# Optimization experiments

Hardware: AMD Instinct MI355X
Metric: run time of the kernel (lower is better)

Reference implementation:

```python
import jax, jax.numpy as jnp
import numpy as np

EMBED = 1024
HEADS = 8
HEAD_DIM = EMBED // HEADS
WINDOW = 128
B, T = 2, 2048


def setup_inputs() -> dict:
    key = jax.random.key(0)
    ks = jax.random.split(key, 6)
    s_in = 1.0 / np.sqrt(EMBED)
    return {
        "x": jax.random.normal(ks[0], (B, T, EMBED), dtype=jnp.float32),
        "W_qkv": jax.random.normal(ks[1], (EMBED, 3 * EMBED), dtype=jnp.float32) * s_in,
        "b_qkv": jax.random.normal(ks[2], (3 * EMBED,), dtype=jnp.float32) * 0.01,
        "W_proj": jax.random.normal(ks[3], (EMBED, EMBED), dtype=jnp.float32) * s_in,
        "b_proj": jax.random.normal(ks[4], (EMBED,), dtype=jnp.float32) * 0.01,
        "gate": jnp.ones((EMBED,), dtype=jnp.float32),
    }


def reference(x, W_qkv, b_qkv, W_proj, b_proj, gate):
    Bb, Tt, C = x.shape
    qkv = x @ W_qkv + b_qkv                       # [B,T,3C]
    q, k, v = jnp.split(qkv, 3, axis=-1)
    # [B,H,T,D]
    q = q.reshape(Bb, Tt, HEADS, HEAD_DIM).transpose(0, 2, 1, 3)
    k = k.reshape(Bb, Tt, HEADS, HEAD_DIM).transpose(0, 2, 1, 3)
    v = v.reshape(Bb, Tt, HEADS, HEAD_DIM).transpose(0, 2, 1, 3)
    scale = 1.0 / np.sqrt(HEAD_DIM).astype(np.float32)
    att = jnp.einsum('bhqd,bhkd->bhqk', q, k) * scale
    idx = jnp.arange(Tt)
    # causal AND within |i-j| <= window  (diagonal always valid -> no all-masked rows)
    mask = (idx[:, None] >= idx[None, :]) & (jnp.abs(idx[:, None] - idx[None, :]) <= WINDOW)
    att = jnp.where(mask[None, None], att, -jnp.inf)
    att = jax.nn.softmax(att, axis=-1)
    out = jnp.einsum('bhqk,bhkd->bhqd', att, v)
    out = out.transpose(0, 2, 1, 3).reshape(Bb, Tt, C)
    return (out * gate) @ W_proj + b_proj
```

## Files before the change

### kernel.cpp

```cpp
#include <hip/hip_runtime.h>

typedef unsigned short u16;
typedef unsigned int u32;
typedef __attribute__((ext_vector_type(4))) float f32x4;
typedef __attribute__((ext_vector_type(8))) short bf16x8;
typedef __attribute__((ext_vector_type(8))) unsigned short u16x8;

#define SEQ   2048
#define NB    2
#define NH    8
#define HD    128
#define EMB   1024
#define WIN   128
#define MTOT  4096
#define NQKV  3072
#define HSZ   (SEQ*HD)
#define QKVSZ (NB*NH*HSZ)

static __device__ __forceinline__ u16 f2bf(float f){
  u32 x = __builtin_bit_cast(u32, f);
  x += 0x7fffu + ((x >> 16) & 1u);
  return (u16)(x >> 16);
}

static __device__ __forceinline__ void gload_lds16(const void* g, void* l){
  __builtin_amdgcn_global_load_lds((__attribute__((address_space(1))) void*)(void*)(g),
                                   (__attribute__((address_space(3))) void*)(l), 16, 0, 0);
}


__global__ __launch_bounds__(256) void cvt_bf16(const float* __restrict__ in,
                                                u16* __restrict__ out, int n){
  int i = (blockIdx.x * 256 + threadIdx.x) * 8;
  const int stride = gridDim.x * 256 * 8;
  for (; i < n; i += stride){
    float4 a = *(const float4*)(in + i);
    float4 b = *(const float4*)(in + i + 4);
    uint4 o;
    o.x = (u32)f2bf(a.x) | ((u32)f2bf(a.y) << 16);
    o.y = (u32)f2bf(a.z) | ((u32)f2bf(a.w) << 16);
    o.z = (u32)f2bf(b.x) | ((u32)f2bf(b.y) << 16);
    o.w = (u32)f2bf(b.z) | ((u32)f2bf(b.w) << 16);
    *(uint4*)(out + i) = o;
  }
}

__global__ __launch_bounds__(256) void transpose_cvt(const float* __restrict__ in,
                                                     u16* __restrict__ out, int R, int C){
  __shared__ float tile[32][33];
  const int bx = blockIdx.x * 32;
  const int by = blockIdx.y * 32;
  const int tx = threadIdx.x & 31, ty = threadIdx.x >> 5;
  #pragma unroll
  for (int i = 0; i < 32; i += 8)
    tile[ty + i][tx] = in[(size_t)(by + ty + i) * C + bx + tx];
  __syncthreads();
  #pragma unroll
  for (int i = 0; i < 32; i += 8)
    out[(size_t)(bx + ty + i) * R + by + tx] = f2bf(tile[tx][ty + i]);
}


template<int EPIL>
__global__ __launch_bounds__(256) void gemm_bf16(
    const u16* __restrict__ A,
    const u16* __restrict__ Bt,
    const float* __restrict__ bias,
    u16* __restrict__ obf,
    float* __restrict__ of)
{
  constexpr int K = 1024, BK = 64;
  __shared__ u16 As[128 * 64];
  __shared__ u16 Bs[128 * 64];
  const int tid = threadIdx.x, lane = tid & 63, wave = tid >> 6;
  const int m0 = blockIdx.y * 128, n0 = blockIdx.x * 128;
  const int wr = (wave >> 1) * 64, wc = (wave & 1) * 64;

  const int srow = lane >> 3;
  const int scol = ((((lane & 7) << 4) ^ (srow << 4)) >> 1);
  const u16* ag = A  + (size_t)(m0 + wave * 32 + srow) * K + scol;
  const u16* bg = Bt + (size_t)(n0 + wave * 32 + srow) * K + scol;
  u16* al = &As[wave * 32 * 64];
  u16* bl = &Bs[wave * 32 * 64];

  f32x4 acc[4][4] = {};

  for (int kt = 0; kt < K / BK; ++kt){
    #pragma unroll
    for (int j = 0; j < 4; ++j){
      gload_lds16(ag + (size_t)j * 8 * K + kt * BK, al + j * 8 * 64);
      gload_lds16(bg + (size_t)j * 8 * K + kt * BK, bl + j * 8 * 64);
    }
    __syncthreads();
    #pragma unroll
    for (int ks = 0; ks < 2; ++ks){
      const int fr = lane & 15;
      const int colb = ((ks << 6) + ((lane >> 4) << 4)) ^ ((lane & 7) << 4);
      bf16x8 af[4], bfr[4];
      #pragma unroll
      for (int mi = 0; mi < 4; ++mi)
        af[mi] = *(const bf16x8*)((const char*)As + (wr + mi * 16 + fr) * 128 + colb);
      #pragma unroll
      for (int ni = 0; ni < 4; ++ni)
        bfr[ni] = *(const bf16x8*)((const char*)Bs + (wc + ni * 16 + fr) * 128 + colb);
      #pragma unroll
      for (int mi = 0; mi < 4; ++mi)
        #pragma unroll
        for (int ni = 0; ni < 4; ++ni)
          acc[mi][ni] = __builtin_amdgcn_mfma_f32_16x16x32_bf16(af[mi], bfr[ni], acc[mi][ni], 0, 0, 0);
    }
    __syncthreads();
  }

  #pragma unroll
  for (int mi = 0; mi < 4; ++mi){
    const int rg = m0 + wr + mi * 16 + ((lane >> 4) << 2);
    #pragma unroll
    for (int ni = 0; ni < 4; ++ni){
      const int cg = n0 + wc + ni * 16 + (lane & 15);
      const float bs = bias[cg];
      if constexpr (EPIL == 0){
        const int which = cg >> 10, hm = cg & 1023;
        const int b = rg >> 11, t = rg & 2047;
        u16* dst = obf + (size_t)which * QKVSZ
                       + ((size_t)(b * NH + (hm >> 7)) * SEQ + t) * HD + (hm & 127);
        #pragma unroll
        for (int j = 0; j < 4; ++j)
          dst[(size_t)j * HD] = f2bf(acc[mi][ni][j] + bs);
      } else {
        #pragma unroll
        for (int j = 0; j < 4; ++j)
          of[(size_t)(rg + j) * EMB + cg] = acc[mi][ni][j] + bs;
      }
    }
  }
}


__global__ __launch_bounds__(256) void attn_kernel(
    const u16* __restrict__ QKVb, const float* __restrict__ gate, u16* __restrict__ Ao)
{
  __shared__ float S[64 * 196];
  __shared__ u16 KV[128 * 72];
  const int tid = threadIdx.x, lane = tid & 63, wave = tid >> 6;
  const int q0 = blockIdx.x * 64;
  const int bh = blockIdx.y;
  const u16* Qg = QKVb + (size_t)bh * HSZ;
  const u16* Kg = QKVb + (size_t)QKVSZ + (size_t)bh * HSZ;
  const u16* Vg = QKVb + (size_t)2 * QKVSZ + (size_t)bh * HSZ;
  const int kstart = q0 - WIN;

  bf16x8 qf[4];
  {
    const u16* qp = Qg + (size_t)(q0 + wave * 16 + (lane & 15)) * HD + 8 * (lane >> 4);
    #pragma unroll
    for (int ks = 0; ks < 4; ++ks) qf[ks] = *(const bf16x8*)(qp + ks * 32);
  }
  const float scale = 0.08838834764831845f;

  for (int c = 0; c < 3; ++c){
    {
      const int keyl = tid >> 2;
      int krow = kstart + c * 64 + keyl;
      krow = min(max(krow, 0), SEQ - 1);
      const u16* kp = Kg + (size_t)krow * HD + (tid & 3) * 8;
      u16* ksh = &KV[keyl * 136 + (tid & 3) * 8];
      #pragma unroll
      for (int r = 0; r < 4; ++r)
        *(uint4*)(ksh + r * 32) = *(const uint4*)(kp + r * 32);
    }
    __syncthreads();
    f32x4 sacc[4] = {};
    #pragma unroll
    for (int ks = 0; ks < 4; ++ks){
      #pragma unroll
      for (int nf = 0; nf < 4; ++nf){
        bf16x8 kf = *(const bf16x8*)(&KV[(nf * 16 + (lane & 15)) * 136 + ks * 32 + 8 * (lane >> 4)]);
        sacc[nf] = __builtin_amdgcn_mfma_f32_16x16x32_bf16(qf[ks], kf, sacc[nf], 0, 0, 0);
      }
    }
    #pragma unroll
    for (int nf = 0; nf < 4; ++nf){
      const int kc = c * 64 + nf * 16 + (lane & 15);
      const int kg = kstart + kc;
      #pragma unroll
      for (int j = 0; j < 4; ++j){
        const int qr = wave * 16 + ((lane >> 4) << 2) + j;
        const int qg = q0 + qr;
        const bool ok = (kg >= 0) && (kg <= qg) && (qg - kg <= WIN);
        S[qr * 196 + kc] = ok ? sacc[nf][j] * scale : -1e30f;
      }
    }
    __syncthreads();
  }

  {
    const int r = tid >> 2, sub = tid & 3;
    float4 v[12];
    float mx = -1e30f;
    #pragma unroll
    for (int i = 0; i < 12; ++i){
      v[i] = *(const float4*)(&S[r * 196 + (sub + 4 * i) * 4]);
      mx = fmaxf(mx, fmaxf(fmaxf(v[i].x, v[i].y), fmaxf(v[i].z, v[i].w)));
    }
    mx = fmaxf(mx, __shfl_xor(mx, 1));
    mx = fmaxf(mx, __shfl_xor(mx, 2));
    float sum = 0.f;
    #pragma unroll
    for (int i = 0; i < 12; ++i){
      v[i].x = __expf(v[i].x - mx); v[i].y = __expf(v[i].y - mx);
      v[i].z = __expf(v[i].z - mx); v[i].w = __expf(v[i].w - mx);
      sum += v[i].x + v[i].y + v[i].z + v[i].w;
    }
    sum += __shfl_xor(sum, 1);
    sum += __shfl_xor(sum, 2);
    const float inv = 1.0f / sum;
    #pragma unroll
    for (int i = 0; i < 12; ++i){
      v[i].x *= inv; v[i].y *= inv; v[i].z *= inv; v[i].w *= inv;
      *(float4*)(&S[r * 196 + (sub + 4 * i) * 4]) = v[i];
    }
  }
  __syncthreads();

  f32x4 oacc[8] = {};
  for (int c = 0; c < 3; ++c){
    {
      const int keyl = tid & 63;
      int krow = kstart + c * 64 + keyl;
      krow = min(max(krow, 0), SEQ - 1);
      const u16* vp = Vg + (size_t)krow * HD + (tid >> 6) * 32;
      #pragma unroll
      for (int r2 = 0; r2 < 4; ++r2){
        u16x8 vv = *(const u16x8*)(vp + r2 * 8);
        const int dbase = (tid >> 6) * 32 + r2 * 8;
        #pragma unroll
        for (int j = 0; j < 8; ++j)
          KV[(dbase + j) * 72 + keyl] = vv[j];
      }
    }
    __syncthreads();
    #pragma unroll
    for (int ks = 0; ks < 2; ++ks){
      const float* sp = &S[(wave * 16 + (lane & 15)) * 196 + c * 64 + ks * 32 + 8 * (lane >> 4)];
      float4 p0 = *(const float4*)sp;
      float4 p1 = *(const float4*)(sp + 4);
      bf16x8 pf;
      pf[0] = (short)f2bf(p0.x); pf[1] = (short)f2bf(p0.y);
      pf[2] = (short)f2bf(p0.z); pf[3] = (short)f2bf(p0.w);
      pf[4] = (short)f2bf(p1.x); pf[5] = (short)f2bf(p1.y);
      pf[6] = (short)f2bf(p1.z); pf[7] = (short)f2bf(p1.w);
      #pragma unroll
      for (int nf = 0; nf < 8; ++nf){
        bf16x8 vf = *(const bf16x8*)(&KV[(nf * 16 + (lane & 15)) * 72 + ks * 32 + 8 * (lane >> 4)]);
        oacc[nf] = __builtin_amdgcn_mfma_f32_16x16x32_bf16(pf, vf, oacc[nf], 0, 0, 0);
      }
    }
    __syncthreads();
  }

  {
    const int b = bh >> 3, h = bh & 7;
    #pragma unroll
    for (int nf = 0; nf < 8; ++nf){
      const int d = nf * 16 + (lane & 15);
      const float gv = gate[h * HD + d];
      #pragma unroll
      for (int j = 0; j < 4; ++j){
        const int t = q0 + wave * 16 + ((lane >> 4) << 2) + j;
        Ao[((size_t)(b * SEQ + t)) * EMB + h * HD + d] = f2bf(oacc[nf][j] * gv);
      }
    }
  }
}


extern "C" void kernel_launch(void* const* d_in, const int* in_sizes, int n_in,
                              void* d_out, int out_size, void* d_ws, size_t ws_size,
                              hipStream_t stream)
{
  const float* x     = (const float*)d_in[0];
  const float* Wqkv  = (const float*)d_in[1];
  const float* bqkv  = (const float*)d_in[2];
  const float* Wproj = (const float*)d_in[3];
  const float* bproj = (const float*)d_in[4];
  const float* gate  = (const float*)d_in[5];
  float* out = (float*)d_out;

  u16* Xb   = (u16*)d_ws;
  u16* Wqt  = Xb   + (size_t)MTOT * EMB;
  u16* Wpt  = Wqt  + (size_t)NQKV * EMB;
  u16* QKVb = Wpt  + (size_t)EMB * EMB;
  u16* Ao   = QKVb + (size_t)3 * QKVSZ;

  cvt_bf16<<<dim3(2048), dim3(256), 0, stream>>>(x, Xb, MTOT * EMB);
  transpose_cvt<<<dim3(NQKV / 32, EMB / 32), dim3(256), 0, stream>>>(Wqkv, Wqt, EMB, NQKV);
  transpose_cvt<<<dim3(EMB / 32, EMB / 32), dim3(256), 0, stream>>>(Wproj, Wpt, EMB, EMB);

  gemm_bf16<0><<<dim3(NQKV / 128, MTOT / 128), dim3(256), 0, stream>>>(
      Xb, Wqt, bqkv, QKVb, (float*)nullptr);

  attn_kernel<<<dim3(SEQ / 64, NB * NH), dim3(256), 0, stream>>>(QKVb, gate, Ao);

  gemm_bf16<1><<<dim3(EMB / 128, MTOT / 128), dim3(256), 0, stream>>>(
      Ao, Wpt, bproj, (u16*)nullptr, out);
}
```

Before: 157.4 us.

## Replace QKV GEMM with 256x256 tiled, 8-wave, double-buffered pipelined kernel

Adds a dedicated QKV projection GEMM that uses 256x256 output tiles with 512 threads. Global-to-LDS loads are double-buffered and interleaved with MFMA phases, using explicit vmcnt waits, barriers and setprio. A grouped block-index swizzle is added for L2 locality. The goal is to raise data reuse per tile and overlap memory with compute in the largest GEMM. The cost is 128 KB of LDS per block and only 192 workgroups, which may underfill the GPU's compute units and risks ordering bugs in the hand-scheduled pipeline.

```diff
diff --git a/kernel.cpp b/kernel.cpp
--- a/kernel.cpp
+++ b/kernel.cpp
@@ -27,6 +27,8 @@
   __builtin_amdgcn_global_load_lds((__attribute__((address_space(1))) void*)(void*)(g),
                                    (__attribute__((address_space(3))) void*)(l), 16, 0, 0);
 }
+
+#define VMW(n) asm volatile("s_waitcnt vmcnt(" #n ")" ::: "memory")
 
 
 __global__ __launch_bounds__(256) void cvt_bf16(const float* __restrict__ in,
@@ -61,12 +63,130 @@
 }
 
 
-template<int EPIL>
-__global__ __launch_bounds__(256) void gemm_bf16(
+#define SLOTB 32768
+
+__global__ __launch_bounds__(512, 2) void gemm256_qkv(
     const u16* __restrict__ A,
     const u16* __restrict__ Bt,
     const float* __restrict__ bias,
-    u16* __restrict__ obf,
+    u16* __restrict__ obf)
+{
+  constexpr int K = 1024;
+  constexpr int NIT = K / 128;
+  __shared__ char sm[131072];
+  char* smA = sm;
+  char* smB = sm + 2 * SLOTB;
+
+  const int tid = threadIdx.x, lane = tid & 63, w = tid >> 6;
+  const int wr = w >> 2, wc = w & 3;
+  const int fr = lane & 15, hk = lane >> 4;
+
+  const int nwg = 16 * 12;
+  const int bid = blockIdx.x;
+  const int swz = (bid & 7) * (nwg >> 3) + (bid >> 3);
+  const int bx = swz % 12, by = swz / 12;
+  const int m0 = by * 256, n0 = bx * 256;
+
+  const int srow = lane >> 3;
+  const int scol = (((lane & 7) ^ srow) << 3);
+  const u16* ag = A  + (size_t)(m0 + w * 8 + srow) * K + scol;
+  const u16* bg = Bt + (size_t)(n0 + w * 8 + srow) * K + scol;
+
+  auto STG = [&](int slot, int abm, int h, int kt){
+    const u16* s = (abm ? bg : ag) + (size_t)h * 128 * K + kt * 64;
+    char* d = (abm ? smB : smA) + slot * SLOTB + h * 16384 + w * 1024;
+    gload_lds16(s, d);
+    gload_lds16(s + 64 * K, d + 8192);
+  };
+
+  auto LDA = [&](int slot, int mh, int mi, int ks) -> bf16x8 {
+    const int r = wr * 128 + mh * 64 + mi * 16 + fr;
+    const int cb = (ks * 64 + hk * 16) ^ ((r & 7) << 4);
+    return *(const bf16x8*)(smA + slot * SLOTB + r * 128 + cb);
+  };
+  auto LDB = [&](int slot, int nh, int ni, int ks) -> bf16x8 {
+    const int r = wc * 64 + nh * 32 + ni * 16 + fr;
+    const int cb = (ks * 64 + hk * 16) ^ ((r & 7) << 4);
+    return *(const bf16x8*)(smB + slot * SLOTB + r * 128 + cb);
+  };
+
+  bf16x8 a[4][2], b[2][2][2];
+  f32x4 acc[8][4] = {};
+
+  auto RDA = [&](int slot, int mh){
+    #pragma unroll
+    for (int mi = 0; mi < 4; ++mi)
+      #pragma unroll
+      for (int ks = 0; ks < 2; ++ks) a[mi][ks] = LDA(slot, mh, mi, ks);
+  };
+  auto RDB = [&](int slot, int nh){
+    #pragma unroll
+    for (int ni = 0; ni < 2; ++ni)
+      #pragma unroll
+      for (int ks = 0; ks < 2; ++ks) b[nh][ni][ks] = LDB(slot, nh, ni, ks);
+  };
+  auto MF = [&](int mh, int nh){
+    __builtin_amdgcn_s_setprio(1);
+    #pragma unroll
+    for (int mi = 0; mi < 4; ++mi)
+      #pragma unroll
+      for (int ni = 0; ni < 2; ++ni)
+        #pragma unroll
+        for (int ks = 0; ks < 2; ++ks)
+          acc[mh * 4 + mi][nh * 2 + ni] = __builtin_amdgcn_mfma_f32_16x16x32_bf16(
+              a[mi][ks], b[nh][ni][ks], acc[mh * 4 + mi][nh * 2 + ni], 0, 0, 0);
+    __builtin_amdgcn_s_setprio(0);
+  };
+  auto BAR = [&](){
+    asm volatile("" ::: "memory");
+    __builtin_amdgcn_s_barrier();
+    asm volatile("" ::: "memory");
+  };
+
+  STG(0, 0, 0, 0); STG(0, 0, 1, 0); STG(0, 1, 0, 0); STG(0, 1, 1, 0);
+  STG(1, 0, 0, 1);
+  VMW(2);
+  BAR();
+
+  for (int i = 0; i < NIT; ++i){
+    const int k1 = 2 * i + 1;
+    const int k2 = (2 * i + 2) & 15;
+    const int k3 = (2 * i + 3) & 15;
+    RDA(0, 0); RDB(0, 0); STG(1, 0, 1, k1); BAR(); MF(0, 0); BAR();
+    RDB(0, 1); STG(1, 1, 0, k1); BAR(); MF(0, 1); BAR();
+    RDA(0, 1); STG(1, 1, 1, k1); BAR(); MF(1, 1); BAR();
+    STG(0, 0, 0, k2); BAR(); MF(1, 0); VMW(2); BAR();
+    RDA(1, 0); RDB(1, 0); STG(0, 0, 1, k2); BAR(); MF(0, 0); BAR();
+    RDB(1, 1); STG(0, 1, 0, k2); BAR(); MF(0, 1); BAR();
+    RDA(1, 1); STG(0, 1, 1, k2); BAR(); MF(1, 1); BAR();
+    STG(1, 0, 0, k3); BAR(); MF(1, 0); VMW(2); BAR();
+  }
+
+  VMW(0);
+
+  #pragma unroll
+  for (int mi = 0; mi < 8; ++mi){
+    const int rg = m0 + wr * 128 + mi * 16 + (hk << 2);
+    const int b_ = rg >> 11, t = rg & 2047;
+    #pragma unroll
+    for (int ni = 0; ni < 4; ++ni){
+      const int cg = n0 + wc * 64 + ni * 16 + fr;
+      const float bs = bias[cg];
+      const int which = cg >> 10, hm = cg & 1023;
+      u16* dst = obf + (size_t)which * QKVSZ
+                     + ((size_t)(b_ * NH + (hm >> 7)) * SEQ + t) * HD + (hm & 127);
+      #pragma unroll
+      for (int j = 0; j < 4; ++j)
+        dst[(size_t)j * HD] = f2bf(acc[mi][ni][j] + bs);
+    }
+  }
+}
+
+
+__global__ __launch_bounds__(256) void gemm_proj(
+    const u16* __restrict__ A,
+    const u16* __restrict__ Bt,
+    const float* __restrict__ bias,
     float* __restrict__ of)
 {
   constexpr int K = 1024, BK = 64;
@@ -119,19 +239,9 @@
     for (int ni = 0; ni < 4; ++ni){
       const int cg = n0 + wc + ni * 16 + (lane & 15);
       const float bs = bias[cg];
-      if constexpr (EPIL == 0){
-        const int which = cg >> 10, hm = cg & 1023;
-        const int b = rg >> 11, t = rg & 2047;
-        u16* dst = obf + (size_t)which * QKVSZ
-                       + ((size_t)(b * NH + (hm >> 7)) * SEQ + t) * HD + (hm & 127);
-        #pragma unroll
-        for (int j = 0; j < 4; ++j)
-          dst[(size_t)j * HD] = f2bf(acc[mi][ni][j] + bs);
-      } else {
-        #pragma unroll
-        for (int j = 0; j < 4; ++j)
-          of[(size_t)(rg + j) * EMB + cg] = acc[mi][ni][j] + bs;
-      }
+      #pragma unroll
+      for (int j = 0; j < 4; ++j)
+        of[(size_t)(rg + j) * EMB + cg] = acc[mi][ni][j] + bs;
     }
   }
 }
@@ -297,11 +407,9 @@
   transpose_cvt<<<dim3(NQKV / 32, EMB / 32), dim3(256), 0, stream>>>(Wqkv, Wqt, EMB, NQKV);
   transpose_cvt<<<dim3(EMB / 32, EMB / 32), dim3(256), 0, stream>>>(Wproj, Wpt, EMB, EMB);
 
-  gemm_bf16<0><<<dim3(NQKV / 128, MTOT / 128), dim3(256), 0, stream>>>(
-      Xb, Wqt, bqkv, QKVb, (float*)nullptr);
+  gemm256_qkv<<<dim3(16 * 12), dim3(512), 0, stream>>>(Xb, Wqt, bqkv, QKVb);
 
   attn_kernel<<<dim3(SEQ / 64, NB * NH), dim3(256), 0, stream>>>(QKVb, gate, Ao);
 
-  gemm_bf16<1><<<dim3(EMB / 128, MTOT / 128), dim3(256), 0, stream>>>(
-      Ao, Wpt, bproj, (u16*)nullptr, out);
-}
+  gemm_proj<<<dim3(EMB / 128, MTOT / 128), dim3(256), 0, stream>>>(Ao, Wpt, bproj, out);
+}
```

New measurement: 158.3 us. Within noise of the previous version (+0.6%).
